# Kernel optimization log

Hardware: AMD Instinct MI355X
Metric: run time of the kernel (lower is better)

The kernel has to match this reference:

```python
import jax, jax.numpy as jnp
import numpy as np

# ---- hyperparameters (from init_kwargs) ----
SIGMA, RHO = 1.0, 10.0
ALPHA, BETA = 1.0, 1.0
K = 3  # ksize; patches are non-overlapping KxK, structure tensor computed on each patch
GRAY_W = np.array([0.2989, 0.587, 0.114], dtype=np.float32)  # torchvision Grayscale weights


def _gauss1d(sigma):
    d = np.arange(-1.0, 2.0, dtype=np.float32)  # radius-1 kernel (fits 3x3 patches)
    g = np.exp(-d * d / (2.0 * sigma * sigma))
    return (g / g.sum()).astype(np.float32)


def _dgauss1d(sigma):
    d = np.arange(-1.0, 2.0, dtype=np.float32)
    g = _gauss1d(sigma)
    return (-d / (sigma * sigma) * g).astype(np.float32)


def _conv3(x, k2d):
    # 'same' zero-padded 3x3 correlation over the last two dims, fully broadcast
    H, W = x.shape[-2], x.shape[-1]
    xp = jnp.pad(x, [(0, 0)] * (x.ndim - 2) + [(1, 1), (1, 1)])
    out = jnp.zeros_like(x)
    for i in range(3):
        for j in range(3):
            out = out + k2d[i, j] * xp[..., i:i + H, j:j + W]
    return out


# precomputed separable kernels (numpy constants)
_G_S, _DG_S, _G_R = _gauss1d(SIGMA), _dgauss1d(SIGMA), _gauss1d(RHO)
_KX = np.outer(_G_S, _DG_S)   # d/dx (last axis), gaussian-smoothed
_KY = np.outer(_DG_S, _G_S)   # d/dy
_KS = np.outer(_G_R, _G_R)    # rho smoothing


def _structure_tensor(gray):
    # gray: (..., K, K) -> (..., 3, K, K) components (Jxx, Jyy, Jxy)
    Ix = _conv3(gray, _KX)
    Iy = _conv3(gray, _KY)
    Jxx = _conv3(Ix * Ix, _KS)
    Jyy = _conv3(Iy * Iy, _KS)
    Jxy = _conv3(Ix * Iy, _KS)
    return jnp.stack([Jxx, Jyy, Jxy], axis=-3)


def _compute_patches(img):
    # img: (B, 3, H, W) -> (B, P, 3*K*K); non-overlapping KxK patches,
    # grayscale -> structure tensor -> per-patch L2 normalize (vectorized, no vmap-of-tiny-ops)
    B, C, H, W = img.shape
    Hb, Wb = H // K, W // K
    p = img.reshape(B, C, Hb, K, Wb, K).transpose(0, 2, 4, 1, 3, 5)  # (B,Hb,Wb,3,K,K)
    p = p.reshape(B, Hb * Wb, C, K, K)
    gray = jnp.einsum('bpchw,c->bphw', p, jnp.asarray(GRAY_W, p.dtype))
    st = _structure_tensor(gray)                                      # (B,P,3,K,K)
    n = jnp.sqrt(jnp.sum(st * st, axis=(-3, -2, -1), keepdims=True)) + 1e-12
    st = st / n
    return st.reshape(B, Hb * Wb, 3 * K * K)


def _resize(img, factor):
    B, C, H, W = img.shape
    return jax.image.resize(img, (B, C, int(H * factor), int(W * factor)),
                            method='bicubic', antialias=False)


def _pairdist_sq(a, b):
    # squared L2 pairwise distance (monotone in L2; only used for argmin)
    aa = jnp.sum(a * a, axis=-1)[:, :, None]
    bb = jnp.sum(b * b, axis=-1)[:, None, :]
    ab = jnp.einsum('bnw,bmw->bnm', a, b)
    return aa + bb - 2.0 * ab


def _loss(x, gt):
    p1 = _compute_patches(x)
    p2 = _compute_patches(gt)
    p2_2 = _compute_patches(_resize(gt, 0.5))
    p2_4 = _compute_patches(_resize(gt, 0.25))
    p2c = jnp.concatenate([p2, p2_2, p2_4], axis=1)      # (B, P2cat, 27)
    score = ALPHA * _pairdist_sq(p1, p2c) + BETA * _pairdist_sq(p2, p2c)
    ind = jnp.argmin(score, axis=2)                      # (B, P1) nearest-neighbor indices
    sel = jnp.take_along_axis(p2c, ind[:, :, None], axis=1)
    return jnp.mean(jnp.abs(p1 - sel))                   # L1 criterion


def setup_inputs() -> dict:
    key = jax.random.key(0)
    k1, k2 = jax.random.split(key)
    x = jax.random.uniform(k1, (4, 3, 192, 192), dtype=jnp.float32)
    gt = jax.random.uniform(k2, (4, 3, 192, 192), dtype=jnp.float32)
    return {'x': x, 'gt': gt}


def reference(x, gt):
    return _loss(x, gt)
```

## Files before the change

### kernel.cpp

```cpp
#include <hip/hip_runtime.h>
#include <hip/hip_bf16.h>
#include <math.h>

namespace {
constexpr int BATCH = 4;
constexpr int IMG   = 192;
constexpr int NP1   = 4096;
constexpr int MALL  = 5376;
constexpr int RS    = 28;
constexpr int NCHUNK = 16;
constexpr int TPC    = 21;

#define GA 0.27406862f
#define GB 0.45186276f
#define RC 0.33277732f
#define RD 0.33444537f

typedef __bf16 bf16x8 __attribute__((ext_vector_type(8)));
typedef float  f32x4  __attribute__((ext_vector_type(4)));

__device__ __forceinline__ void conv3(const float in[9], const float k[9], float out[9]) {
#pragma unroll
  for (int y = 0; y < 3; ++y)
#pragma unroll
    for (int x = 0; x < 3; ++x) {
      float s = 0.f;
#pragma unroll
      for (int i = 0; i < 3; ++i) {
        int yy = y + i - 1;
        if (yy < 0 || yy > 2) continue;
#pragma unroll
        for (int j = 0; j < 3; ++j) {
          int xx = x + j - 1;
          if (xx < 0 || xx > 2) continue;
          s = fmaf(k[i * 3 + j], in[yy * 3 + xx], s);
        }
      }
      out[y * 3 + x] = s;
    }
}

__device__ __forceinline__ void mkw(int k0, int IS, float w[4], int k[4]) {
  const float W4[4] = {-0.0625f, 0.5625f, 0.5625f, -0.0625f};
  float ssum = 0.f;
#pragma unroll
  for (int u = 0; u < 4; ++u) {
    int kk = k0 + u;
    bool v = (kk >= 0) && (kk < IS);
    w[u] = v ? W4[u] : 0.f;
    k[u] = v ? kk : 0;
    ssum += w[u];
  }
  float inv = 1.f / ssum;
#pragma unroll
  for (int u = 0; u < 4; ++u) w[u] *= inv;
}

__global__ void resize_kernel(const float* __restrict__ src, float* __restrict__ dst,
                              int OS, int step, int koff) {
  int o = blockIdx.x * blockDim.x + threadIdx.x;
  int total = BATCH * 3 * OS * OS;
  if (o >= total) return;
  int j = o % OS;
  int i = (o / OS) % OS;
  int bc = o / (OS * OS);
  const float* s = src + (size_t)bc * IMG * IMG;
  float wr[4], wc[4];
  int kr[4], kc[4];
  mkw(step * i + koff, IMG, wr, kr);
  mkw(step * j + koff, IMG, wc, kc);
  float acc = 0.f;
#pragma unroll
  for (int u = 0; u < 4; ++u) {
    const float* srow = s + (size_t)kr[u] * IMG;
    float rsum = 0.f;
#pragma unroll
    for (int v = 0; v < 4; ++v) rsum = fmaf(wc[v], srow[kc[v]], rsum);
    acc = fmaf(wr[u], rsum, acc);
  }
  dst[o] = acc;
}

template <bool WRITE_C>
__global__ void patch_kernel(const float* __restrict__ img, int H, int Wb,
                             float* __restrict__ dst, int dstBstride, int dstOff,
                             int npp) {
  int g = blockIdx.x * blockDim.x + threadIdx.x;
  if (g >= BATCH * npp) return;
  int b = g / npp, p = g - b * npp;
  int hb = p / Wb, wb = p - hb * Wb;
  const size_t plane = (size_t)H * H;
  const float* base = img + (size_t)b * 3 * plane + (size_t)(hb * 3) * H + wb * 3;

  float gray[9];
#pragma unroll
  for (int y = 0; y < 3; ++y)
#pragma unroll
    for (int x = 0; x < 3; ++x) {
      float r  = base[(size_t)y * H + x];
      float gg = base[plane + (size_t)y * H + x];
      float bl = base[2 * plane + (size_t)y * H + x];
      gray[y * 3 + x] = fmaf(0.114f, bl, fmaf(0.587f, gg, 0.2989f * r));
    }

  const float KX[9] = {GA * GA, 0.f, -GA * GA, GB * GA, 0.f, -GB * GA, GA * GA, 0.f, -GA * GA};
  const float KY[9] = {GA * GA, GA * GB, GA * GA, 0.f, 0.f, 0.f, -GA * GA, -GA * GB, -GA * GA};
  const float KS[9] = {RC * RC, RC * RD, RC * RC, RD * RC, RD * RD, RD * RC, RC * RC, RC * RD, RC * RC};

  float Ix[9], Iy[9];
  conv3(gray, KX, Ix);
  conv3(gray, KY, Iy);
  float Pxx[9], Pyy[9], Pxy[9];
#pragma unroll
  for (int t = 0; t < 9; ++t) {
    Pxx[t] = Ix[t] * Ix[t];
    Pyy[t] = Iy[t] * Iy[t];
    Pxy[t] = Ix[t] * Iy[t];
  }
  float st[27];
  conv3(Pxx, KS, st + 0);
  conv3(Pyy, KS, st + 9);
  conv3(Pxy, KS, st + 18);

  float s2 = 0.f;
#pragma unroll
  for (int d = 0; d < 27; ++d) s2 = fmaf(st[d], st[d], s2);
  float nrm = sqrtf(s2) + 1e-12f;
  float inv = 1.0f / nrm;

  float* orow = dst + ((size_t)b * dstBstride + dstOff + p) * RS;
  float cs = 0.f;
#pragma unroll
  for (int d = 0; d < 27; ++d) {
    float v = st[d] * inv;
    orow[d] = v;
    cs = fmaf(v, v, cs);
  }
  if (WRITE_C) orow[27] = cs;
}

__global__ void pack_kernel(const float* __restrict__ p1, const float* __restrict__ p2c,
                            unsigned* __restrict__ Qp, unsigned* __restrict__ Cp) {
  int g = blockIdx.x * 256 + threadIdx.x;
  const int NC = BATCH * MALL;
  float v[28];
  unsigned* dst;
  if (g < NC) {
    const float* s = p2c + (size_t)g * RS;
#pragma unroll
    for (int d = 0; d < 27; ++d) v[d] = s[d];
    v[27] = -s[27];
    dst = Cp + (size_t)g * 32;
  } else {
    int q = g - NC;
    if (q >= BATCH * NP1) return;
    int b = q >> 12, n = q & (NP1 - 1);
    const float* a = p1 + (size_t)q * RS;
    const float* c = p2c + ((size_t)b * MALL + n) * RS;
#pragma unroll
    for (int d = 0; d < 27; ++d) v[d] = a[d] + c[d];
    v[27] = 1.0f;
    dst = Qp + (size_t)q * 32;
  }

  unsigned uh[16], ul[16];
#pragma unroll
  for (int p = 0; p < 16; ++p) {
    float a  = (2 * p < 28) ? v[2 * p] : 0.f;
    float bb = (2 * p + 1 < 28) ? v[2 * p + 1] : 0.f;
    __hip_bfloat16 ah = __float2bfloat16(a);
    __hip_bfloat16 bh = __float2bfloat16(bb);
    float af = __bfloat162float(ah), bf2 = __bfloat162float(bh);
    __hip_bfloat16 al = __float2bfloat16(a - af);
    __hip_bfloat16 bl = __float2bfloat16(bb - bf2);
    uh[p] = ((unsigned)__builtin_bit_cast(unsigned short, bh) << 16) |
            (unsigned)__builtin_bit_cast(unsigned short, ah);
    ul[p] = ((unsigned)__builtin_bit_cast(unsigned short, bl) << 16) |
            (unsigned)__builtin_bit_cast(unsigned short, al);
  }
  uint4* d4 = reinterpret_cast<uint4*>(dst);
  d4[0] = make_uint4(uh[0], uh[1], uh[2], uh[3]);
  d4[1] = make_uint4(uh[4], uh[5], uh[6], uh[7]);
  d4[2] = make_uint4(uh[8], uh[9], uh[10], uh[11]);
  d4[3] = make_uint4(uh[12], uh[13], uh[14], uh[15]);
  d4[4] = make_uint4(ul[0], ul[1], ul[2], ul[3]);
  d4[5] = make_uint4(ul[4], ul[5], ul[6], ul[7]);
  d4[6] = make_uint4(ul[8], ul[9], ul[10], ul[11]);
  d4[7] = make_uint4(ul[12], ul[13], ul[14], ul[15]);
}

__global__ void __launch_bounds__(256, 4) argmin_mfma_kernel(
    const unsigned* __restrict__ Qp, const unsigned* __restrict__ Cp,
    float* __restrict__ pscore, int* __restrict__ pidx) {
  const int lane = threadIdx.x & 63;
  const int w = threadIdx.x >> 6;
  const int chunk = blockIdx.y;
  const int b = blockIdx.z;
  const int nbase = blockIdx.x * 256 + w * 64;
  const int lm = lane & 15, lg = lane >> 4;

  bf16x8 qh[4], ql[4];
#pragma unroll
  for (int t = 0; t < 4; ++t) {
    const unsigned* rp = Qp + ((size_t)(b * NP1 + nbase + t * 16 + lm)) * 32 + lg * 4;
    qh[t] = *reinterpret_cast<const bf16x8*>(rp);
    ql[t] = *reinterpret_cast<const bf16x8*>(rp + 16);
  }

  float best[4][4];
  int idx[4][4];
#pragma unroll
  for (int t = 0; t < 4; ++t)
#pragma unroll
    for (int r = 0; r < 4; ++r) { best[t][r] = -INFINITY; idx[t][r] = 0; }

  const int tile0 = chunk * TPC;
  for (int i = 0; i < TPC; ++i) {
    const int m0 = (tile0 + i) * 16;
    const unsigned* cr = Cp + ((size_t)(b * MALL + m0 + lm)) * 32 + lg * 4;
    bf16x8 ch = *reinterpret_cast<const bf16x8*>(cr);
    bf16x8 cl = *reinterpret_cast<const bf16x8*>(cr + 16);
    const int mi = m0 + lm;
#pragma unroll
    for (int t = 0; t < 4; ++t) {
      f32x4 a = {0.f, 0.f, 0.f, 0.f};
      a = __builtin_amdgcn_mfma_f32_16x16x32_bf16(qh[t], ch, a, 0, 0, 0);
      a = __builtin_amdgcn_mfma_f32_16x16x32_bf16(ql[t], ch, a, 0, 0, 0);
      a = __builtin_amdgcn_mfma_f32_16x16x32_bf16(qh[t], cl, a, 0, 0, 0);
#pragma unroll
      for (int r = 0; r < 4; ++r) {
        bool g = a[r] > best[t][r];
        best[t][r] = g ? a[r] : best[t][r];
        idx[t][r] = g ? mi : idx[t][r];
      }
    }
  }

#pragma unroll
  for (int t = 0; t < 4; ++t)
#pragma unroll
    for (int r = 0; r < 4; ++r) {
      float bv = best[t][r];
      int bi = idx[t][r];
#pragma unroll
      for (int mk = 1; mk < 16; mk <<= 1) {
        float ov = __shfl_xor(bv, mk, 64);
        int oi = __shfl_xor(bi, mk, 64);
        bool take = (ov > bv) || (ov == bv && oi < bi);
        bv = take ? ov : bv;
        bi = take ? oi : bi;
      }
      if (lm == 0) {
        int row = nbase + t * 16 + lg * 4 + r;
        size_t o = ((size_t)(b * NP1 + row)) * NCHUNK + chunk;
        pscore[o] = bv;
        pidx[o] = bi;
      }
    }
}

__global__ void finalize_kernel(const float* __restrict__ p1, const float* __restrict__ p2c,
                                const float* __restrict__ pscore, const int* __restrict__ pidx,
                                float* __restrict__ bsum) {
  int g = blockIdx.x * 256 + threadIdx.x;
  float bt = -INFINITY;
  int bi = 0;
  for (int ms = 0; ms < NCHUNK; ++ms) {
    float s = pscore[(size_t)g * NCHUNK + ms];
    int ix = pidx[(size_t)g * NCHUNK + ms];
    bool gg = (s > bt) || (s == bt && ix < bi);
    bt = gg ? s : bt;
    bi = gg ? ix : bi;
  }
  int b = g >> 12;
  const float* a = p1 + (size_t)g * RS;
  const float* s2 = p2c + ((size_t)b * MALL + bi) * RS;
  float acc = 0.f;
#pragma unroll
  for (int d = 0; d < 27; ++d) acc += fabsf(a[d] - s2[d]);

  __shared__ float red[256];
  red[threadIdx.x] = acc;
  __syncthreads();
  for (int st = 128; st > 0; st >>= 1) {
    if (threadIdx.x < st) red[threadIdx.x] += red[threadIdx.x + st];
    __syncthreads();
  }
  if (threadIdx.x == 0) bsum[blockIdx.x] = red[0];
}

__global__ void final_sum_kernel(const float* __restrict__ bsum, float* __restrict__ out) {
  __shared__ float red[64];
  red[threadIdx.x] = bsum[threadIdx.x];
  __syncthreads();
  for (int st = 32; st > 0; st >>= 1) {
    if (threadIdx.x < st) red[threadIdx.x] += red[threadIdx.x + st];
    __syncthreads();
  }
  if (threadIdx.x == 0) out[0] = red[0] * (1.0f / 442368.0f);
}

}

extern "C" void kernel_launch(void* const* d_in, const int* in_sizes, int n_in,
                              void* d_out, int out_size, void* d_ws, size_t ws_size,
                              hipStream_t stream) {
  const float* x  = (const float*)d_in[0];
  const float* gt = (const float*)d_in[1];
  float* out = (float*)d_out;

  float* ws = (float*)d_ws;
  float* p1   = ws;
  float* p2c  = p1 + (size_t)BATCH * NP1 * RS;
  float* r96  = p2c + (size_t)BATCH * MALL * RS;
  float* r48  = r96 + (size_t)BATCH * 3 * 96 * 96;
  unsigned* Qp = (unsigned*)(r48 + (size_t)BATCH * 3 * 48 * 48);
  unsigned* Cp = Qp + (size_t)BATCH * NP1 * 32;
  float* pscore = (float*)(Cp + (size_t)BATCH * MALL * 32);
  int*   pidx   = (int*)(pscore + (size_t)BATCH * NP1 * NCHUNK);
  float* bsum   = (float*)(pidx + (size_t)BATCH * NP1 * NCHUNK);

  {
    int tot = BATCH * 3 * 96 * 96;
    resize_kernel<<<(tot + 255) / 256, 256, 0, stream>>>(gt, r96, 96, 2, -1);
  }
  {
    int tot = BATCH * 3 * 48 * 48;
    resize_kernel<<<(tot + 255) / 256, 256, 0, stream>>>(gt, r48, 48, 4, 0);
  }

  patch_kernel<false><<<(BATCH * NP1 + 255) / 256, 256, 0, stream>>>(
      x, IMG, 64, p1, NP1, 0, NP1);
  patch_kernel<true><<<(BATCH * NP1 + 255) / 256, 256, 0, stream>>>(
      gt, IMG, 64, p2c, MALL, 0, NP1);
  patch_kernel<true><<<(BATCH * 1024 + 255) / 256, 256, 0, stream>>>(
      r96, 96, 32, p2c, MALL, NP1, 1024);
  patch_kernel<true><<<(BATCH * 256 + 255) / 256, 256, 0, stream>>>(
      r48, 48, 16, p2c, MALL, NP1 + 1024, 256);

  {
    int tot = BATCH * (MALL + NP1);
    pack_kernel<<<(tot + 255) / 256, 256, 0, stream>>>(p1, p2c, Qp, Cp);
  }

  {
    dim3 grid(16, NCHUNK, BATCH);
    argmin_mfma_kernel<<<grid, 256, 0, stream>>>(Qp, Cp, pscore, pidx);
  }

  finalize_kernel<<<(BATCH * NP1) / 256, 256, 0, stream>>>(p1, p2c, pscore, pidx, bsum);
  final_sum_kernel<<<1, 64, 0, stream>>>(bsum, out);
}
```

Before: 73.88 us.

## Fuse resize, patch and pack stages into one prep kernel; fold final sum

Merges the two bicubic resize kernels, four patch kernels and the pack kernel into a single prep kernel. It computes grayscale bicubic samples on the fly and writes both fp32 rows and the bf16 hi/lo packed rows directly. The final sum kernel is folded into finalize through an atomic last-block counter, cutting the launch count from 10 to 3 and dropping the intermediate resized images. The cost is redundant bicubic reads per patch pixel, a heavier kernel with more register pressure, and a counter that is reset inside prep.

```diff
diff --git a/kernel.cpp b/kernel.cpp
--- a/kernel.cpp
+++ b/kernel.cpp
@@ -5,7 +5,10 @@
 namespace {
 constexpr int BATCH = 4;
 constexpr int IMG   = 192;
+constexpr int PL    = IMG * IMG;
 constexpr int NP1   = 4096;
+constexpr int N96   = 1024;
+constexpr int N48   = 256;
 constexpr int MALL  = 5376;
 constexpr int RS    = 28;
 constexpr int NCHUNK = 16;
@@ -38,6 +41,36 @@
       }
       out[y * 3 + x] = s;
     }
+}
+
+__device__ __forceinline__ void st_from_gray(const float gray[9], float stv[27], float& cs) {
+  const float KX[9] = {GA * GA, 0.f, -GA * GA, GB * GA, 0.f, -GB * GA, GA * GA, 0.f, -GA * GA};
+  const float KY[9] = {GA * GA, GA * GB, GA * GA, 0.f, 0.f, 0.f, -GA * GA, -GA * GB, -GA * GA};
+  const float KS[9] = {RC * RC, RC * RD, RC * RC, RD * RC, RD * RD, RD * RC, RC * RC, RC * RD, RC * RC};
+  float Ix[9], Iy[9];
+  conv3(gray, KX, Ix);
+  conv3(gray, KY, Iy);
+  float Pxx[9], Pyy[9], Pxy[9];
+#pragma unroll
+  for (int t = 0; t < 9; ++t) {
+    Pxx[t] = Ix[t] * Ix[t];
+    Pyy[t] = Iy[t] * Iy[t];
+    Pxy[t] = Ix[t] * Iy[t];
+  }
+  conv3(Pxx, KS, stv + 0);
+  conv3(Pyy, KS, stv + 9);
+  conv3(Pxy, KS, stv + 18);
+  float s2 = 0.f;
+#pragma unroll
+  for (int d = 0; d < 27; ++d) s2 = fmaf(stv[d], stv[d], s2);
+  float inv = 1.0f / (sqrtf(s2) + 1e-12f);
+  float c = 0.f;
+#pragma unroll
+  for (int d = 0; d < 27; ++d) {
+    stv[d] *= inv;
+    c = fmaf(stv[d], stv[d], c);
+  }
+  cs = c;
 }
 
 __device__ __forceinline__ void mkw(int k0, int IS, float w[4], int k[4]) {
@@ -56,15 +89,8 @@
   for (int u = 0; u < 4; ++u) w[u] *= inv;
 }
 
-__global__ void resize_kernel(const float* __restrict__ src, float* __restrict__ dst,
-                              int OS, int step, int koff) {
-  int o = blockIdx.x * blockDim.x + threadIdx.x;
-  int total = BATCH * 3 * OS * OS;
-  if (o >= total) return;
-  int j = o % OS;
-  int i = (o / OS) % OS;
-  int bc = o / (OS * OS);
-  const float* s = src + (size_t)bc * IMG * IMG;
+__device__ __forceinline__ float bicubic_gray(const float* __restrict__ im,
+                                              int i, int j, int step, int koff) {
   float wr[4], wc[4];
   int kr[4], kc[4];
   mkw(step * i + koff, IMG, wr, kr);
@@ -72,97 +98,22 @@
   float acc = 0.f;
 #pragma unroll
   for (int u = 0; u < 4; ++u) {
-    const float* srow = s + (size_t)kr[u] * IMG;
-    float rsum = 0.f;
-#pragma unroll
-    for (int v = 0; v < 4; ++v) rsum = fmaf(wc[v], srow[kc[v]], rsum);
-    acc = fmaf(wr[u], rsum, acc);
-  }
-  dst[o] = acc;
-}
-
-template <bool WRITE_C>
-__global__ void patch_kernel(const float* __restrict__ img, int H, int Wb,
-                             float* __restrict__ dst, int dstBstride, int dstOff,
-                             int npp) {
-  int g = blockIdx.x * blockDim.x + threadIdx.x;
-  if (g >= BATCH * npp) return;
-  int b = g / npp, p = g - b * npp;
-  int hb = p / Wb, wb = p - hb * Wb;
-  const size_t plane = (size_t)H * H;
-  const float* base = img + (size_t)b * 3 * plane + (size_t)(hb * 3) * H + wb * 3;
-
-  float gray[9];
-#pragma unroll
-  for (int y = 0; y < 3; ++y)
-#pragma unroll
-    for (int x = 0; x < 3; ++x) {
-      float r  = base[(size_t)y * H + x];
-      float gg = base[plane + (size_t)y * H + x];
-      float bl = base[2 * plane + (size_t)y * H + x];
-      gray[y * 3 + x] = fmaf(0.114f, bl, fmaf(0.587f, gg, 0.2989f * r));
-    }
-
-  const float KX[9] = {GA * GA, 0.f, -GA * GA, GB * GA, 0.f, -GB * GA, GA * GA, 0.f, -GA * GA};
-  const float KY[9] = {GA * GA, GA * GB, GA * GA, 0.f, 0.f, 0.f, -GA * GA, -GA * GB, -GA * GA};
-  const float KS[9] = {RC * RC, RC * RD, RC * RC, RD * RC, RD * RD, RD * RC, RC * RC, RC * RD, RC * RC};
-
-  float Ix[9], Iy[9];
-  conv3(gray, KX, Ix);
-  conv3(gray, KY, Iy);
-  float Pxx[9], Pyy[9], Pxy[9];
-#pragma unroll
-  for (int t = 0; t < 9; ++t) {
-    Pxx[t] = Ix[t] * Ix[t];
-    Pyy[t] = Iy[t] * Iy[t];
-    Pxy[t] = Ix[t] * Iy[t];
-  }
-  float st[27];
-  conv3(Pxx, KS, st + 0);
-  conv3(Pyy, KS, st + 9);
-  conv3(Pxy, KS, st + 18);
-
-  float s2 = 0.f;
-#pragma unroll
-  for (int d = 0; d < 27; ++d) s2 = fmaf(st[d], st[d], s2);
-  float nrm = sqrtf(s2) + 1e-12f;
-  float inv = 1.0f / nrm;
-
-  float* orow = dst + ((size_t)b * dstBstride + dstOff + p) * RS;
-  float cs = 0.f;
-#pragma unroll
-  for (int d = 0; d < 27; ++d) {
-    float v = st[d] * inv;
-    orow[d] = v;
-    cs = fmaf(v, v, cs);
-  }
-  if (WRITE_C) orow[27] = cs;
-}
-
-__global__ void pack_kernel(const float* __restrict__ p1, const float* __restrict__ p2c,
-                            unsigned* __restrict__ Qp, unsigned* __restrict__ Cp) {
-  int g = blockIdx.x * 256 + threadIdx.x;
-  const int NC = BATCH * MALL;
-  float v[28];
-  unsigned* dst;
-  if (g < NC) {
-    const float* s = p2c + (size_t)g * RS;
-#pragma unroll
-    for (int d = 0; d < 27; ++d) v[d] = s[d];
-    v[27] = -s[27];
-    dst = Cp + (size_t)g * 32;
-  } else {
-    int q = g - NC;
-    if (q >= BATCH * NP1) return;
-    int b = q >> 12, n = q & (NP1 - 1);
-    const float* a = p1 + (size_t)q * RS;
-    const float* c = p2c + ((size_t)b * MALL + n) * RS;
-#pragma unroll
-    for (int d = 0; d < 27; ++d) v[d] = a[d] + c[d];
-    v[27] = 1.0f;
-    dst = Qp + (size_t)q * 32;
-  }
-
+    float rs = 0.f;
+#pragma unroll
+    for (int v = 0; v < 4; ++v) {
+      int o = kr[u] * IMG + kc[v];
+      float r  = im[o];
+      float g2 = im[PL + o];
+      float bl = im[2 * PL + o];
+      float gy = fmaf(0.114f, bl, fmaf(0.587f, g2, 0.2989f * r));
+      rs = fmaf(wc[v], gy, rs);
+    }
+    acc = fmaf(wr[u], rs, acc);
+  }
+  return acc;
+}
+
+__device__ __forceinline__ void pack_row(const float v[28], unsigned* __restrict__ dst) {
   unsigned uh[16], ul[16];
 #pragma unroll
   for (int p = 0; p < 16; ++p) {
@@ -189,6 +140,115 @@
   d4[7] = make_uint4(ul[12], ul[13], ul[14], ul[15]);
 }
 
+__device__ __forceinline__ void store_row28(float* __restrict__ dst, const float v[28]) {
+  float4* d4 = reinterpret_cast<float4*>(dst);
+#pragma unroll
+  for (int i = 0; i < 7; ++i)
+    d4[i] = make_float4(v[4 * i], v[4 * i + 1], v[4 * i + 2], v[4 * i + 3]);
+}
+
+__global__ void __launch_bounds__(256) prep_kernel(
+    const float* __restrict__ x, const float* __restrict__ gt,
+    float* __restrict__ p1, float* __restrict__ p2c,
+    unsigned* __restrict__ Qp, unsigned* __restrict__ Cp,
+    unsigned* __restrict__ ctr) {
+  int g = blockIdx.x * 256 + threadIdx.x;
+  if (g == 0) ctr[0] = 0;
+
+  if (g < BATCH * NP1) {
+    int b = g >> 12, p = g & (NP1 - 1);
+    int hb = p >> 6, wb = p & 63;
+    const size_t boff = (size_t)b * 3 * PL + (size_t)(hb * 3) * IMG + wb * 3;
+
+    float gr[9];
+    const float* bx = x + boff;
+#pragma unroll
+    for (int y = 0; y < 3; ++y)
+#pragma unroll
+      for (int xx = 0; xx < 3; ++xx) {
+        int o = y * IMG + xx;
+        gr[y * 3 + xx] = fmaf(0.114f, bx[2 * PL + o], fmaf(0.587f, bx[PL + o], 0.2989f * bx[o]));
+      }
+    float s1[28];
+    float cs1;
+    st_from_gray(gr, s1, cs1);
+    s1[27] = cs1;
+
+    const float* bg = gt + boff;
+#pragma unroll
+    for (int y = 0; y < 3; ++y)
+#pragma unroll
+      for (int xx = 0; xx < 3; ++xx) {
+        int o = y * IMG + xx;
+        gr[y * 3 + xx] = fmaf(0.114f, bg[2 * PL + o], fmaf(0.587f, bg[PL + o], 0.2989f * bg[o]));
+      }
+    float s2[28];
+    float cs2;
+    st_from_gray(gr, s2, cs2);
+    s2[27] = cs2;
+
+    store_row28(p1 + (size_t)g * RS, s1);
+    size_t crow = (size_t)b * MALL + p;
+    store_row28(p2c + crow * RS, s2);
+
+    float vc[28];
+#pragma unroll
+    for (int d = 0; d < 27; ++d) vc[d] = s2[d];
+    vc[27] = -cs2;
+    pack_row(vc, Cp + crow * 32);
+
+    float vq[28];
+#pragma unroll
+    for (int d = 0; d < 27; ++d) vq[d] = s1[d] + s2[d];
+    vq[27] = 1.0f;
+    pack_row(vq, Qp + (size_t)g * 32);
+  } else if (g < BATCH * (NP1 + N96)) {
+    int q = g - BATCH * NP1;
+    int b = q >> 10, p = q & (N96 - 1);
+    int hb = p >> 5, wb = p & 31;
+    const float* im = gt + (size_t)b * 3 * PL;
+    float gr[9];
+#pragma unroll
+    for (int y = 0; y < 3; ++y)
+#pragma unroll
+      for (int xx = 0; xx < 3; ++xx)
+        gr[y * 3 + xx] = bicubic_gray(im, 3 * hb + y, 3 * wb + xx, 2, -1);
+    float s[28];
+    float cs;
+    st_from_gray(gr, s, cs);
+    s[27] = cs;
+    size_t crow = (size_t)b * MALL + NP1 + p;
+    store_row28(p2c + crow * RS, s);
+    float vc[28];
+#pragma unroll
+    for (int d = 0; d < 27; ++d) vc[d] = s[d];
+    vc[27] = -cs;
+    pack_row(vc, Cp + crow * 32);
+  } else if (g < BATCH * (NP1 + N96 + N48)) {
+    int q = g - BATCH * (NP1 + N96);
+    int b = q >> 8, p = q & (N48 - 1);
+    int hb = p >> 4, wb = p & 15;
+    const float* im = gt + (size_t)b * 3 * PL;
+    float gr[9];
+#pragma unroll
+    for (int y = 0; y < 3; ++y)
+#pragma unroll
+      for (int xx = 0; xx < 3; ++xx)
+        gr[y * 3 + xx] = bicubic_gray(im, 3 * hb + y, 3 * wb + xx, 4, 0);
+    float s[28];
+    float cs;
+    st_from_gray(gr, s, cs);
+    s[27] = cs;
+    size_t crow = (size_t)b * MALL + NP1 + N96 + p;
+    store_row28(p2c + crow * RS, s);
+    float vc[28];
+#pragma unroll
+    for (int d = 0; d < 27; ++d) vc[d] = s[d];
+    vc[27] = -cs;
+    pack_row(vc, Cp + crow * 32);
+  }
+}
+
 __global__ void __launch_bounds__(256, 4) argmin_mfma_kernel(
     const unsigned* __restrict__ Qp, const unsigned* __restrict__ Cp,
     float* __restrict__ pscore, int* __restrict__ pidx) {
@@ -259,9 +319,10 @@
     }
 }
 
-__global__ void finalize_kernel(const float* __restrict__ p1, const float* __restrict__ p2c,
-                                const float* __restrict__ pscore, const int* __restrict__ pidx,
-                                float* __restrict__ bsum) {
+__global__ void __launch_bounds__(256) finalize_kernel(
+    const float* __restrict__ p1, const float* __restrict__ p2c,
+    const float* __restrict__ pscore, const int* __restrict__ pidx,
+    float* __restrict__ bsum, unsigned* __restrict__ ctr, float* __restrict__ out) {
   int g = blockIdx.x * 256 + threadIdx.x;
   float bt = -INFINITY;
   int bi = 0;
@@ -286,18 +347,16 @@
     if (threadIdx.x < st) red[threadIdx.x] += red[threadIdx.x + st];
     __syncthreads();
   }
-  if (threadIdx.x == 0) bsum[blockIdx.x] = red[0];
-}
-
-__global__ void final_sum_kernel(const float* __restrict__ bsum, float* __restrict__ out) {
-  __shared__ float red[64];
-  red[threadIdx.x] = bsum[threadIdx.x];
-  __syncthreads();
-  for (int st = 32; st > 0; st >>= 1) {
-    if (threadIdx.x < st) red[threadIdx.x] += red[threadIdx.x + st];
-    __syncthreads();
-  }
-  if (threadIdx.x == 0) out[0] = red[0] * (1.0f / 442368.0f);
+  if (threadIdx.x == 0) {
+    __hip_atomic_store(&bsum[blockIdx.x], red[0], __ATOMIC_RELEASE, __HIP_MEMORY_SCOPE_AGENT);
+    unsigned prev = __hip_atomic_fetch_add(ctr, 1u, __ATOMIC_ACQ_REL, __HIP_MEMORY_SCOPE_AGENT);
+    if (prev == 63) {
+      float s = 0.f;
+      for (int i = 0; i < 64; ++i)
+        s += __hip_atomic_load(&bsum[i], __ATOMIC_ACQUIRE, __HIP_MEMORY_SCOPE_AGENT);
+      out[0] = s * (1.0f / 442368.0f);
+    }
+  }
 }
 
 }
@@ -312,35 +371,16 @@
   float* ws = (float*)d_ws;
   float* p1   = ws;
   float* p2c  = p1 + (size_t)BATCH * NP1 * RS;
-  float* r96  = p2c + (size_t)BATCH * MALL * RS;
-  float* r48  = r96 + (size_t)BATCH * 3 * 96 * 96;
-  unsigned* Qp = (unsigned*)(r48 + (size_t)BATCH * 3 * 48 * 48);
+  unsigned* Qp = (unsigned*)(p2c + (size_t)BATCH * MALL * RS);
   unsigned* Cp = Qp + (size_t)BATCH * NP1 * 32;
   float* pscore = (float*)(Cp + (size_t)BATCH * MALL * 32);
   int*   pidx   = (int*)(pscore + (size_t)BATCH * NP1 * NCHUNK);
   float* bsum   = (float*)(pidx + (size_t)BATCH * NP1 * NCHUNK);
+  unsigned* ctr = (unsigned*)(bsum + 64);
 
   {
-    int tot = BATCH * 3 * 96 * 96;
-    resize_kernel<<<(tot + 255) / 256, 256, 0, stream>>>(gt, r96, 96, 2, -1);
-  }
-  {
-    int tot = BATCH * 3 * 48 * 48;
-    resize_kernel<<<(tot + 255) / 256, 256, 0, stream>>>(gt, r48, 48, 4, 0);
-  }
-
-  patch_kernel<false><<<(BATCH * NP1 + 255) / 256, 256, 0, stream>>>(
-      x, IMG, 64, p1, NP1, 0, NP1);
-  patch_kernel<true><<<(BATCH * NP1 + 255) / 256, 256, 0, stream>>>(
-      gt, IMG, 64, p2c, MALL, 0, NP1);
-  patch_kernel<true><<<(BATCH * 1024 + 255) / 256, 256, 0, stream>>>(
-      r96, 96, 32, p2c, MALL, NP1, 1024);
-  patch_kernel<true><<<(BATCH * 256 + 255) / 256, 256, 0, stream>>>(
-      r48, 48, 16, p2c, MALL, NP1 + 1024, 256);
-
-  {
-    int tot = BATCH * (MALL + NP1);
-    pack_kernel<<<(tot + 255) / 256, 256, 0, stream>>>(p1, p2c, Qp, Cp);
+    int tot = BATCH * (NP1 + N96 + N48);
+    prep_kernel<<<tot / 256, 256, 0, stream>>>(x, gt, p1, p2c, Qp, Cp, ctr);
   }
 
   {
@@ -348,6 +388,5 @@
     argmin_mfma_kernel<<<grid, 256, 0, stream>>>(Qp, Cp, pscore, pidx);
   }
 
-  finalize_kernel<<<(BATCH * NP1) / 256, 256, 0, stream>>>(p1, p2c, pscore, pidx, bsum);
-  final_sum_kernel<<<1, 64, 0, stream>>>(bsum, out);
-}
+  finalize_kernel<<<(BATCH * NP1) / 256, 256, 0, stream>>>(p1, p2c, pscore, pidx, bsum, ctr, out);
+}
```

Result: no change. 74.75 us (+1.2%).

## Pack argmin score and tile index into one uint key, retile operand layout

Applied to the files above, without the earlier changes.

Operands are now stored pre-swizzled in 16-row MFMA fragment order, so each lane reads a contiguous, fully coalesced 16-byte chunk. The inner loop biases the accumulator by 4 so scores stay positive, then packs the score bits with the tile index in the low 5 bits into a single unsigned key. A plain unsigned max replaces the float compare plus two selects. This trims VALU work and register use per MFMA tile, at the cost of truncating the low 5 mantissa bits, which can alter tie-breaking between near-equal candidates. Launch bounds are also lowered from 4 to 2 blocks per SIMD.

```diff
diff --git a/kernel.cpp b/kernel.cpp
--- a/kernel.cpp
+++ b/kernel.cpp
@@ -5,7 +5,10 @@
 namespace {
 constexpr int BATCH = 4;
 constexpr int IMG   = 192;
+constexpr int PL    = IMG * IMG;
 constexpr int NP1   = 4096;
+constexpr int N96   = 1024;
+constexpr int N48   = 256;
 constexpr int MALL  = 5376;
 constexpr int RS    = 28;
 constexpr int NCHUNK = 16;
@@ -144,13 +147,15 @@
   int g = blockIdx.x * 256 + threadIdx.x;
   const int NC = BATCH * MALL;
   float v[28];
-  unsigned* dst;
+  unsigned* base;
+  int rl;
   if (g < NC) {
     const float* s = p2c + (size_t)g * RS;
 #pragma unroll
     for (int d = 0; d < 27; ++d) v[d] = s[d];
     v[27] = -s[27];
-    dst = Cp + (size_t)g * 32;
+    base = Cp + (size_t)(g >> 4) * 512;
+    rl = g & 15;
   } else {
     int q = g - NC;
     if (q >= BATCH * NP1) return;
@@ -160,7 +165,8 @@
 #pragma unroll
     for (int d = 0; d < 27; ++d) v[d] = a[d] + c[d];
     v[27] = 1.0f;
-    dst = Qp + (size_t)q * 32;
+    base = Qp + (size_t)(q >> 4) * 512;
+    rl = q & 15;
   }
 
   unsigned uh[16], ul[16];
@@ -178,20 +184,18 @@
     ul[p] = ((unsigned)__builtin_bit_cast(unsigned short, bl) << 16) |
             (unsigned)__builtin_bit_cast(unsigned short, al);
   }
-  uint4* d4 = reinterpret_cast<uint4*>(dst);
-  d4[0] = make_uint4(uh[0], uh[1], uh[2], uh[3]);
-  d4[1] = make_uint4(uh[4], uh[5], uh[6], uh[7]);
-  d4[2] = make_uint4(uh[8], uh[9], uh[10], uh[11]);
-  d4[3] = make_uint4(uh[12], uh[13], uh[14], uh[15]);
-  d4[4] = make_uint4(ul[0], ul[1], ul[2], ul[3]);
-  d4[5] = make_uint4(ul[4], ul[5], ul[6], ul[7]);
-  d4[6] = make_uint4(ul[8], ul[9], ul[10], ul[11]);
-  d4[7] = make_uint4(ul[12], ul[13], ul[14], ul[15]);
-}
-
-__global__ void __launch_bounds__(256, 4) argmin_mfma_kernel(
+#pragma unroll
+  for (int lg = 0; lg < 4; ++lg) {
+    *reinterpret_cast<uint4*>(base + (size_t)(lg * 16 + rl) * 4) =
+        make_uint4(uh[4 * lg], uh[4 * lg + 1], uh[4 * lg + 2], uh[4 * lg + 3]);
+    *reinterpret_cast<uint4*>(base + 256 + (size_t)(lg * 16 + rl) * 4) =
+        make_uint4(ul[4 * lg], ul[4 * lg + 1], ul[4 * lg + 2], ul[4 * lg + 3]);
+  }
+}
+
+__global__ void __launch_bounds__(256, 2) argmin_mfma_kernel(
     const unsigned* __restrict__ Qp, const unsigned* __restrict__ Cp,
-    float* __restrict__ pscore, int* __restrict__ pidx) {
+    unsigned* __restrict__ pkey, int* __restrict__ pidx) {
   const int lane = threadIdx.x & 63;
   const int w = threadIdx.x >> 6;
   const int chunk = blockIdx.y;
@@ -202,36 +206,34 @@
   bf16x8 qh[4], ql[4];
 #pragma unroll
   for (int t = 0; t < 4; ++t) {
-    const unsigned* rp = Qp + ((size_t)(b * NP1 + nbase + t * 16 + lm)) * 32 + lg * 4;
-    qh[t] = *reinterpret_cast<const bf16x8*>(rp);
-    ql[t] = *reinterpret_cast<const bf16x8*>(rp + 16);
-  }
-
-  float best[4][4];
-  int idx[4][4];
+    const unsigned* tb = Qp + (size_t)((b * NP1 + nbase) >> 4) * 512 + (size_t)t * 512 + lane * 4;
+    qh[t] = *reinterpret_cast<const bf16x8*>(tb);
+    ql[t] = *reinterpret_cast<const bf16x8*>(tb + 256);
+  }
+
+  unsigned keys[4][4];
 #pragma unroll
   for (int t = 0; t < 4; ++t)
 #pragma unroll
-    for (int r = 0; r < 4; ++r) { best[t][r] = -INFINITY; idx[t][r] = 0; }
+    for (int r = 0; r < 4; ++r) keys[t][r] = 0u;
 
   const int tile0 = chunk * TPC;
+  const unsigned* cb = Cp + (size_t)(b * (MALL >> 4) + tile0) * 512 + lane * 4;
   for (int i = 0; i < TPC; ++i) {
-    const int m0 = (tile0 + i) * 16;
-    const unsigned* cr = Cp + ((size_t)(b * MALL + m0 + lm)) * 32 + lg * 4;
-    bf16x8 ch = *reinterpret_cast<const bf16x8*>(cr);
-    bf16x8 cl = *reinterpret_cast<const bf16x8*>(cr + 16);
-    const int mi = m0 + lm;
+    bf16x8 ch = *reinterpret_cast<const bf16x8*>(cb);
+    bf16x8 cl = *reinterpret_cast<const bf16x8*>(cb + 256);
+    cb += 512;
+    const unsigned tag = 31u - (unsigned)i;
 #pragma unroll
     for (int t = 0; t < 4; ++t) {
-      f32x4 a = {0.f, 0.f, 0.f, 0.f};
+      f32x4 a = {4.f, 4.f, 4.f, 4.f};
       a = __builtin_amdgcn_mfma_f32_16x16x32_bf16(qh[t], ch, a, 0, 0, 0);
       a = __builtin_amdgcn_mfma_f32_16x16x32_bf16(ql[t], ch, a, 0, 0, 0);
       a = __builtin_amdgcn_mfma_f32_16x16x32_bf16(qh[t], cl, a, 0, 0, 0);
 #pragma unroll
       for (int r = 0; r < 4; ++r) {
-        bool g = a[r] > best[t][r];
-        best[t][r] = g ? a[r] : best[t][r];
-        idx[t][r] = g ? mi : idx[t][r];
+        unsigned kb = (__builtin_bit_cast(unsigned, (float)a[r]) & 0xFFFFFFE0u) | tag;
+        keys[t][r] = keys[t][r] > kb ? keys[t][r] : kb;
       }
     }
   }
@@ -240,36 +242,36 @@
   for (int t = 0; t < 4; ++t)
 #pragma unroll
     for (int r = 0; r < 4; ++r) {
-      float bv = best[t][r];
-      int bi = idx[t][r];
+      unsigned k = keys[t][r];
+      int m = (tile0 + (int)(31u - (k & 31u))) * 16 + lm;
 #pragma unroll
       for (int mk = 1; mk < 16; mk <<= 1) {
-        float ov = __shfl_xor(bv, mk, 64);
-        int oi = __shfl_xor(bi, mk, 64);
-        bool take = (ov > bv) || (ov == bv && oi < bi);
-        bv = take ? ov : bv;
-        bi = take ? oi : bi;
+        unsigned ok = (unsigned)__shfl_xor((int)k, mk, 64);
+        int om = __shfl_xor(m, mk, 64);
+        bool take = (ok > k) || (ok == k && om < m);
+        k = take ? ok : k;
+        m = take ? om : m;
       }
       if (lm == 0) {
         int row = nbase + t * 16 + lg * 4 + r;
         size_t o = ((size_t)(b * NP1 + row)) * NCHUNK + chunk;
-        pscore[o] = bv;
-        pidx[o] = bi;
+        pkey[o] = k & 0xFFFFFFE0u;
+        pidx[o] = m;
       }
     }
 }
 
 __global__ void finalize_kernel(const float* __restrict__ p1, const float* __restrict__ p2c,
-                                const float* __restrict__ pscore, const int* __restrict__ pidx,
+                                const unsigned* __restrict__ pkey, const int* __restrict__ pidx,
                                 float* __restrict__ bsum) {
   int g = blockIdx.x * 256 + threadIdx.x;
-  float bt = -INFINITY;
+  unsigned bk = 0u;
   int bi = 0;
   for (int ms = 0; ms < NCHUNK; ++ms) {
-    float s = pscore[(size_t)g * NCHUNK + ms];
+    unsigned k = pkey[(size_t)g * NCHUNK + ms];
     int ix = pidx[(size_t)g * NCHUNK + ms];
-    bool gg = (s > bt) || (s == bt && ix < bi);
-    bt = gg ? s : bt;
+    bool gg = k > bk;
+    bk = gg ? k : bk;
     bi = gg ? ix : bi;
   }
   int b = g >> 12;
@@ -316,8 +318,8 @@
   float* r48  = r96 + (size_t)BATCH * 3 * 96 * 96;
   unsigned* Qp = (unsigned*)(r48 + (size_t)BATCH * 3 * 48 * 48);
   unsigned* Cp = Qp + (size_t)BATCH * NP1 * 32;
-  float* pscore = (float*)(Cp + (size_t)BATCH * MALL * 32);
-  int*   pidx   = (int*)(pscore + (size_t)BATCH * NP1 * NCHUNK);
+  unsigned* pkey = (unsigned*)(Cp + (size_t)BATCH * MALL * 32);
+  int*   pidx   = (int*)(pkey + (size_t)BATCH * NP1 * NCHUNK);
   float* bsum   = (float*)(pidx + (size_t)BATCH * NP1 * NCHUNK);
 
   {
@@ -345,9 +347,9 @@
 
   {
     dim3 grid(16, NCHUNK, BATCH);
-    argmin_mfma_kernel<<<grid, 256, 0, stream>>>(Qp, Cp, pscore, pidx);
-  }
-
-  finalize_kernel<<<(BATCH * NP1) / 256, 256, 0, stream>>>(p1, p2c, pscore, pidx, bsum);
+    argmin_mfma_kernel<<<grid, 256, 0, stream>>>(Qp, Cp, pkey, pidx);
+  }
+
+  finalize_kernel<<<(BATCH * NP1) / 256, 256, 0, stream>>>(p1, p2c, pkey, pidx, bsum);
   final_sum_kernel<<<1, 64, 0, stream>>>(bsum, out);
 }
```

After: 60.44 us. 18.2% less time.
